# Optimization experiments

Hardware: AMD Instinct MI355X
Metric: run time of the kernel (lower is better)

## Reference

```python
import jax, jax.numpy as jnp
import numpy as np
import math

B, T, C, H = 2, 4096, 512, 8
HD = C // H


def setup_inputs() -> dict:
    key = jax.random.key(0)
    k1, k2, k3 = jax.random.split(key, 3)
    x = jax.random.normal(k1, (B, T, C), dtype=jnp.float32)
    # weights stored as [in, out] so y = x @ W (equivalent to torch Linear with W^T)
    w_qkv = jax.random.normal(k2, (C, 3 * C), dtype=jnp.float32) * (1.0 / math.sqrt(C))
    w_out = jax.random.normal(k3, (C, C), dtype=jnp.float32) * (1.0 / math.sqrt(C))
    return {"x": x, "w_qkv": w_qkv, "w_out": w_out}


def reference(x, w_qkv, w_out):
    Bs, Ts, Cs = x.shape
    qkv = x @ w_qkv                                   # [B,T,3C]
    q, k, v = jnp.split(qkv, 3, axis=-1)
    # [B,H,T,HD]
    q = q.reshape(Bs, Ts, H, HD).transpose(0, 2, 1, 3)
    k = k.reshape(Bs, Ts, H, HD).transpose(0, 2, 1, 3)
    v = v.reshape(Bs, Ts, H, HD).transpose(0, 2, 1, 3)
    scores = jnp.einsum("bhqd,bhkd->bhqk", q, k) / math.sqrt(HD)
    causal = jnp.tril(jnp.ones((Ts, Ts), dtype=bool))
    scores = jnp.where(causal[None, None], scores, -jnp.inf)
    attn = jax.nn.softmax(scores, axis=-1)            # [B,H,T,T]
    out = jnp.einsum("bhqk,bhkd->bhqd", attn, v)      # [B,H,T,HD]
    out = out.transpose(0, 2, 1, 3).reshape(Bs, Ts, Cs)
    return out @ w_out
```

## Files before the change

kernel.cpp:

```cpp
#include <hip/hip_runtime.h>
#include <hip/hip_bf16.h>

typedef __bf16 bf16;
typedef __bf16 bf16x4 __attribute__((ext_vector_type(4)));
typedef __bf16 bf16x8 __attribute__((ext_vector_type(8)));
typedef float f32x4 __attribute__((ext_vector_type(4)));

#define BB 2
#define TT 4096
#define CC 512
#define HH 8
#define HD 64
#define BHD 16
#define M_TOT 8192

#define SCL (0.125f * 1.44269504f)

#if __has_builtin(__builtin_amdgcn_exp2f)
#define EXP2F(x) __builtin_amdgcn_exp2f(x)
#else
#define EXP2F(x) exp2f(x)
#endif

#define GLDS(gptr, lptr)                                                     \
  __builtin_amdgcn_global_load_lds(                                          \
      (const __attribute__((address_space(1))) void*)(gptr),                 \
      (__attribute__((address_space(3))) void*)(lptr), 16, 0, 0)

__global__ __launch_bounds__(256) void convert_x_kernel(
    const float* __restrict__ X, bf16* __restrict__ Xb) {
  const size_t i0 = ((size_t)blockIdx.x * 256 + threadIdx.x) * 16;
  const float4* p = (const float4*)(X + i0);
#pragma unroll
  for (int c = 0; c < 2; ++c) {
    float4 a = p[c * 2], b = p[c * 2 + 1];
    bf16x8 v;
    v[0] = (bf16)a.x; v[1] = (bf16)a.y; v[2] = (bf16)a.z; v[3] = (bf16)a.w;
    v[4] = (bf16)b.x; v[5] = (bf16)b.y; v[6] = (bf16)b.z; v[7] = (bf16)b.w;
    *(bf16x8*)&Xb[i0 + c * 8] = v;
  }
}

__global__ __launch_bounds__(256) void transpose_w_kernel(
    const float* __restrict__ Wq, const float* __restrict__ Wo,
    bf16* __restrict__ WQT, bf16* __restrict__ WOT) {
  __shared__ float tile[64][65];
  int b = blockIdx.x;
  const float* W; bf16* WT; int N, n0, k0;
  if (b < 192) { W = Wq; WT = WQT; N = 1536; n0 = (b % 24) * 64; k0 = (b / 24) * 64; }
  else { b -= 192; W = Wo; WT = WOT; N = 512; n0 = (b & 7) * 64; k0 = (b >> 3) * 64; }
  const int t = threadIdx.x;
  const int rr = t >> 4, cc4 = (t & 15) * 4;
#pragma unroll
  for (int i = 0; i < 4; ++i) {
    float4 v = *(const float4*)&W[(size_t)(k0 + rr + i * 16) * N + n0 + cc4];
    tile[rr + i * 16][cc4 + 0] = v.x;
    tile[rr + i * 16][cc4 + 1] = v.y;
    tile[rr + i * 16][cc4 + 2] = v.z;
    tile[rr + i * 16][cc4 + 3] = v.w;
  }
  __syncthreads();
#pragma unroll
  for (int i = 0; i < 4; ++i) {
    const int nn = rr + i * 16;
    bf16x4 o;
#pragma unroll
    for (int j = 0; j < 4; ++j) o[j] = (bf16)tile[cc4 + j][nn];
    *(bf16x4*)&WT[(size_t)(n0 + nn) * 512 + k0 + cc4] = o;
  }
}

__global__ __launch_bounds__(256) void gemm_qkv_kernel(
    const bf16* __restrict__ Xb, const bf16* __restrict__ Wt,
    bf16* __restrict__ qw, bf16* __restrict__ kw, bf16* __restrict__ vw) {
  __shared__ __align__(16) bf16 As[128 * 64];
  __shared__ __align__(16) bf16 Bs[128 * 64];
  const int tid = threadIdx.x;
  const int wid = tid >> 6, lane = tid & 63, ln = lane & 15, hi = lane >> 4;
  const int wr = wid >> 1, wc = wid & 1;
  const int m0 = blockIdx.x * 128, n0 = blockIdx.y * 128;
  const int srow = lane >> 3, srcc = (lane & 7) ^ srow;

  f32x4 acc[4][4] = {};

  for (int k0 = 0; k0 < 512; k0 += 64) {
    __syncthreads();
#pragma unroll
    for (int i = 0; i < 4; ++i) {
      const int rb = 32 * wid + 8 * i;
      GLDS(&Xb[(size_t)(m0 + rb + srow) * 512 + k0 + srcc * 8], &As[rb * 64]);
      GLDS(&Wt[(size_t)(n0 + rb + srow) * 512 + k0 + srcc * 8], &Bs[rb * 64]);
    }
    __syncthreads();

    bf16x8 af[4][2], bfr[4][2];
#pragma unroll
    for (int mi = 0; mi < 4; ++mi) {
      const int row = wr * 64 + mi * 16 + ln, rs = row & 7;
      af[mi][0] = *(const bf16x8*)&As[row * 64 + ((hi ^ rs) * 8)];
      af[mi][1] = *(const bf16x8*)&As[row * 64 + (((4 + hi) ^ rs) * 8)];
    }
#pragma unroll
    for (int ni = 0; ni < 4; ++ni) {
      const int row = wc * 64 + ni * 16 + ln, rs = row & 7;
      bfr[ni][0] = *(const bf16x8*)&Bs[row * 64 + ((hi ^ rs) * 8)];
      bfr[ni][1] = *(const bf16x8*)&Bs[row * 64 + (((4 + hi) ^ rs) * 8)];
    }
#pragma unroll
    for (int mi = 0; mi < 4; ++mi)
#pragma unroll
      for (int ni = 0; ni < 4; ++ni) {
        acc[mi][ni] = __builtin_amdgcn_mfma_f32_16x16x32_bf16(af[mi][0], bfr[ni][0], acc[mi][ni], 0, 0, 0);
        acc[mi][ni] = __builtin_amdgcn_mfma_f32_16x16x32_bf16(af[mi][1], bfr[ni][1], acc[mi][ni], 0, 0, 0);
      }
  }

#pragma unroll
  for (int mi = 0; mi < 4; ++mi) {
    int rowb = m0 + wr * 64 + mi * 16 + hi * 4;
    int b = rowb >> 12, t0 = rowb & 4095;
#pragma unroll
    for (int ni = 0; ni < 4; ++ni) {
      int n = n0 + wc * 64 + ni * 16 + ln;
      int which = n >> 9, c = n & 511, h = c >> 6, d = c & 63;
      if (which == 2) {
        bf16x4 pv;
#pragma unroll
        for (int r = 0; r < 4; ++r) pv[r] = (bf16)acc[mi][ni][r];
        const int tb = t0 & 63;
        const int paddr = (((tb >> 4) & 1) << 2) | (((tb >> 2) & 3) << 3) |
                          ((tb >> 5) << 5);
        *(bf16x4*)&vw[((size_t)(b * HH + h) * HD + d) * TT + (t0 & ~63) + paddr] = pv;
      } else {
        bf16* dst = which ? kw : qw;
        const float sc = which ? 1.0f : SCL;
#pragma unroll
        for (int r = 0; r < 4; ++r)
          dst[((size_t)(b * HH + h) * TT + t0 + r) * HD + d] = (bf16)(acc[mi][ni][r] * sc);
      }
    }
  }
}

__global__ __launch_bounds__(512, 4) void attn_piece_kernel(
    const bf16* __restrict__ qw, const bf16* __restrict__ kw,
    const bf16* __restrict__ vt,
    bf16* __restrict__ po, float* __restrict__ pl) {
  __shared__ __align__(16) bf16 Ks[2][64 * 64];
  __shared__ __align__(16) bf16 Vs[2][64 * 64];
  const int tid = threadIdx.x;
  const int wid = tid >> 6, lane = tid & 63, ln = lane & 15, hi = lane >> 4;

  int qb4, bh, chunk;
  {
    const int pid = blockIdx.x;
#define MAPB(OFF, K) { const int l = pid - (OFF);                            \
      qb4 = (2 * (K) - 1) - l / (16 * (K));                                  \
      const int r = l % (16 * (K)); bh = r / (K); chunk = r % (K); }
    if      (pid < 256)  MAPB(0, 8)
    else if (pid < 480)  MAPB(256, 7)
    else if (pid < 672)  MAPB(480, 6)
    else if (pid < 832)  MAPB(672, 5)
    else if (pid < 960)  MAPB(832, 4)
    else if (pid < 1056) MAPB(960, 3)
    else if (pid < 1120) MAPB(1056, 2)
    else                 MAPB(1120, 1)
#undef MAPB
  }
  const int ntot = 4 * qb4 + 4;
  const int t0c = chunk * 8;
  const int t1 = (t0c + 8 < ntot) ? (t0c + 8) : ntot;
  const int pid = blockIdx.x;

  const int q0w = qb4 * 256 + wid * 32;

  const int rbase = 8 * wid + (lane >> 3);
  const int srcch = (lane & 7) ^ (lane >> 3);
  const size_t kb = (size_t)bh * TT * HD, vb = (size_t)bh * HD * TT;

  bf16x8 qf[2][2];
#pragma unroll
  for (int qi = 0; qi < 2; ++qi)
#pragma unroll
    for (int h = 0; h < 2; ++h)
      qf[qi][h] = *(const bf16x8*)&qw[((size_t)bh * TT + q0w + qi * 16 + ln) * HD + h * 32 + hi * 8];

  const bf16* kp[4][2];
#pragma unroll
  for (int kt = 0; kt < 4; ++kt) {
    const int krow = kt * 16 + ln;
    kp[kt][0] = &Ks[0][krow * 64 + ((hi ^ (ln & 7)) * 8)];
    kp[kt][1] = &Ks[0][krow * 64 + (((4 + hi) ^ (ln & 7)) * 8)];
  }
  const bf16* vp[4][2];
#pragma unroll
  for (int db = 0; db < 4; ++db) {
    const int d = db * 16 + ln, rowb = d * 64, dx = d & 7;
#pragma unroll
    for (int h2 = 0; h2 < 2; ++h2)
      vp[db][h2] = &Vs[0][rowb + (((4 * h2 + hi) ^ dx) * 8)];
  }

  f32x4 o[2][4] = {};
  f32x4 osum[2] = {};

  bf16x8 vones;
#pragma unroll
  for (int j = 0; j < 8; ++j) vones[j] = (bf16)1.0f;

  {
    const int kv = t0c * 64;
    GLDS(kw + kb + (size_t)(kv + rbase) * HD + srcch * 8, &Ks[0][(8 * wid) * 64]);
    GLDS(vt + vb + (size_t)rbase * TT + kv + srcch * 8, &Vs[0][(8 * wid) * 64]);
  }
  const bf16* pk0 = kw + kb + (size_t)((t0c + 1) * 64 + rbase) * HD + srcch * 8;
  const bf16* pv0 = vt + vb + (size_t)rbase * TT + (t0c + 1) * 64 + srcch * 8;
  __syncthreads();

#define TILE(t_, BUF) do {                                                   \
    const int kv0 = (t_) * 64;                                               \
    if ((t_) + 1 < t1) {                                                     \
      GLDS(pk0, &Ks[(BUF) ^ 1][(8 * wid) * 64]);                             \
      GLDS(pv0, &Vs[(BUF) ^ 1][(8 * wid) * 64]);                             \
      pk0 += (size_t)64 * HD; pv0 += 64;                                     \
    }                                                                        \
    if (kv0 <= q0w + 31) {                                                   \
      f32x4 s[2][4];                                                         \
      __builtin_amdgcn_s_setprio(1);                                         \
      _Pragma("unroll")                                                      \
      for (int kt = 0; kt < 4; ++kt) {                                       \
        bf16x8 kf0 = *(const bf16x8*)(kp[kt][0] + (BUF) * 4096);             \
        bf16x8 kf1 = *(const bf16x8*)(kp[kt][1] + (BUF) * 4096);             \
        _Pragma("unroll")                                                    \
        for (int qi = 0; qi < 2; ++qi) {                                     \
          f32x4 a = {};                                                      \
          a = __builtin_amdgcn_mfma_f32_16x16x32_bf16(kf0, qf[qi][0], a, 0, 0, 0); \
          a = __builtin_amdgcn_mfma_f32_16x16x32_bf16(kf1, qf[qi][1], a, 0, 0, 0); \
          s[qi][kt] = a;                                                     \
        }                                                                    \
      }                                                                      \
      __builtin_amdgcn_s_setprio(0);                                         \
      _Pragma("unroll")                                                      \
      for (int qi = 0; qi < 2; ++qi) {                                       \
        if (kv0 + 63 > q0w + qi * 16) {                                      \
          const int qg = q0w + qi * 16 + ln;                                 \
          _Pragma("unroll")                                                  \
          for (int kt = 0; kt < 4; ++kt)                                     \
            _Pragma("unroll")                                                \
            for (int r = 0; r < 4; ++r)                                      \
              if (kv0 + kt * 16 + hi * 4 + r > qg) s[qi][kt][r] = -1e30f;    \
        }                                                                    \
      }                                                                      \
      _Pragma("unroll")                                                      \
      for (int qi = 0; qi < 2; ++qi)                                         \
        _Pragma("unroll")                                                    \
        for (int kt = 0; kt < 4; ++kt)                                       \
          _Pragma("unroll")                                                  \
          for (int r = 0; r < 4; ++r) s[qi][kt][r] = EXP2F(s[qi][kt][r]);    \
      bf16x8 pa[2][2];                                                       \
      _Pragma("unroll")                                                      \
      for (int qi = 0; qi < 2; ++qi)                                         \
        _Pragma("unroll")                                                    \
        for (int h2 = 0; h2 < 2; ++h2)                                       \
          _Pragma("unroll")                                                  \
          for (int j = 0; j < 8; ++j)                                        \
            pa[qi][h2][j] = (bf16)s[qi][h2 * 2 + (j >> 2)][j & 3];           \
      __builtin_amdgcn_s_setprio(1);                                         \
      _Pragma("unroll")                                                      \
      for (int qi = 0; qi < 2; ++qi) {                                       \
        osum[qi] = __builtin_amdgcn_mfma_f32_16x16x32_bf16(pa[qi][0], vones, osum[qi], 0, 0, 0); \
        osum[qi] = __builtin_amdgcn_mfma_f32_16x16x32_bf16(pa[qi][1], vones, osum[qi], 0, 0, 0); \
      }                                                                      \
      _Pragma("unroll")                                                      \
      for (int db = 0; db < 4; ++db) {                                       \
        _Pragma("unroll")                                                    \
        for (int h2 = 0; h2 < 2; ++h2) {                                     \
          bf16x8 vf = *(const bf16x8*)(vp[db][h2] + (BUF) * 4096);           \
          _Pragma("unroll")                                                  \
          for (int qi = 0; qi < 2; ++qi)                                     \
            o[qi][db] = __builtin_amdgcn_mfma_f32_16x16x32_bf16(pa[qi][h2], vf, o[qi][db], 0, 0, 0); \
        }                                                                    \
      }                                                                      \
      __builtin_amdgcn_s_setprio(0);                                         \
    }                                                                        \
    __syncthreads();                                                         \
  } while (0)

  int t = t0c;
  for (; t + 1 < t1; t += 2) { TILE(t, 0); TILE(t + 1, 1); }
  if (t < t1) TILE(t, 0);

  {
    bf16* ob = po + (size_t)pid * 16384;
#pragma unroll
    for (int qi = 0; qi < 2; ++qi)
#pragma unroll
      for (int db = 0; db < 4; ++db)
#pragma unroll
        for (int r = 0; r < 4; ++r)
          ob[(wid * 32 + qi * 16 + hi * 4 + r) * 64 + db * 16 + ln] = (bf16)o[qi][db][r];
    if (ln == 0) {
#pragma unroll
      for (int qi = 0; qi < 2; ++qi)
#pragma unroll
        for (int r = 0; r < 4; ++r)
          pl[pid * 256 + wid * 32 + qi * 16 + hi * 4 + r] = osum[qi][r];
    }
  }
#undef TILE
}

__global__ __launch_bounds__(256) void attn_combine_kernel(
    const bf16* __restrict__ po, const float* __restrict__ pl,
    bf16* __restrict__ aw) {
  const int cb = blockIdx.x;
  const int qb4 = 15 - (cb >> 5);
  const int r5 = cb & 31;
  const int bh = r5 >> 1, half = r5 & 1;
  const int tid = threadIdx.x;
  const int q_ = half * 128 + (tid >> 1), dc = (tid & 1) * 32;

  const int k = (qb4 + 2) >> 1;
  static const int OFF[9] = {0, 1120, 1056, 960, 832, 672, 480, 256, 0};
  const int p0 = OFF[k] + ((2 * k - 1) - qb4) * 16 * k + bh * k;

  float sum = 0.f;
  for (int c = 0; c < k; ++c) sum += pl[(p0 + c) * 256 + q_];
  const float inv = 1.0f / sum;

  float acc[32] = {};
  for (int c = 0; c < k; ++c) {
    const bf16* ob = po + (size_t)(p0 + c) * 16384 + q_ * 64 + dc;
#pragma unroll
    for (int cc = 0; cc < 4; ++cc) {
      bf16x8 x = *(const bf16x8*)&ob[cc * 8];
#pragma unroll
      for (int j = 0; j < 8; ++j) acc[cc * 8 + j] += (float)x[j];
    }
  }
  bf16* dst = aw + ((size_t)bh * TT + qb4 * 256 + q_) * 64 + dc;
#pragma unroll
  for (int cc = 0; cc < 4; ++cc) {
    bf16x8 outv;
#pragma unroll
    for (int j = 0; j < 8; ++j) outv[j] = (bf16)(acc[cc * 8 + j] * inv);
    *(bf16x8*)&dst[cc * 8] = outv;
  }
}

__global__ __launch_bounds__(256) void gemm_out_kernel(
    const bf16* __restrict__ A, const bf16* __restrict__ Wot,
    float* __restrict__ out) {
  __shared__ __align__(16) bf16 As[128 * 64];
  __shared__ __align__(16) bf16 Bs[64 * 64];
  const int tid = threadIdx.x;
  const int wid = tid >> 6, lane = tid & 63, ln = lane & 15, hi = lane >> 4;
  const int wr = wid >> 1, wc = wid & 1;
  const int m0 = blockIdx.x * 128, n0 = blockIdx.y * 64;
  const int srow = lane >> 3, srcc = (lane & 7) ^ srow;

  f32x4 acc[4][2] = {};

  for (int k0 = 0; k0 < 512; k0 += 64) {
    const int h = k0 >> 6;
    __syncthreads();
#pragma unroll
    for (int i = 0; i < 4; ++i) {
      const int rb = 32 * wid + 8 * i;
      const int m = m0 + rb + srow;
      const int b = m >> 12, t = m & 4095;
      GLDS(&A[((size_t)(b * HH + h) * TT + t) * HD + srcc * 8], &As[rb * 64]);
    }
#pragma unroll
    for (int i = 0; i < 2; ++i) {
      const int rb = 16 * wid + 8 * i;
      GLDS(&Wot[(size_t)(n0 + rb + srow) * 512 + k0 + srcc * 8], &Bs[rb * 64]);
    }
    __syncthreads();

    bf16x8 af[4][2], bfr[2][2];
#pragma unroll
    for (int mi = 0; mi < 4; ++mi) {
      const int row = wr * 64 + mi * 16 + ln, rs = row & 7;
      af[mi][0] = *(const bf16x8*)&As[row * 64 + ((hi ^ rs) * 8)];
      af[mi][1] = *(const bf16x8*)&As[row * 64 + (((4 + hi) ^ rs) * 8)];
    }
#pragma unroll
    for (int ni = 0; ni < 2; ++ni) {
      const int row = wc * 32 + ni * 16 + ln, rs = row & 7;
      bfr[ni][0] = *(const bf16x8*)&Bs[row * 64 + ((hi ^ rs) * 8)];
      bfr[ni][1] = *(const bf16x8*)&Bs[row * 64 + (((4 + hi) ^ rs) * 8)];
    }
#pragma unroll
    for (int mi = 0; mi < 4; ++mi)
#pragma unroll
      for (int ni = 0; ni < 2; ++ni) {
        acc[mi][ni] = __builtin_amdgcn_mfma_f32_16x16x32_bf16(af[mi][0], bfr[ni][0], acc[mi][ni], 0, 0, 0);
        acc[mi][ni] = __builtin_amdgcn_mfma_f32_16x16x32_bf16(af[mi][1], bfr[ni][1], acc[mi][ni], 0, 0, 0);
      }
  }

#pragma unroll
  for (int mi = 0; mi < 4; ++mi) {
    int rowb = m0 + wr * 64 + mi * 16 + hi * 4;
#pragma unroll
    for (int ni = 0; ni < 2; ++ni) {
      int n = n0 + wc * 32 + ni * 16 + ln;
#pragma unroll
      for (int r = 0; r < 4; ++r)
        out[(size_t)(rowb + r) * 512 + n] = acc[mi][ni][r];
    }
  }
}

extern "C" void kernel_launch(void* const* d_in, const int* in_sizes, int n_in,
                              void* d_out, int out_size, void* d_ws, size_t ws_size,
                              hipStream_t stream) {
  const float* x = (const float*)d_in[0];
  const float* w_qkv = (const float*)d_in[1];
  const float* w_out = (const float*)d_in[2];
  float* out = (float*)d_out;

  const size_t QKV_ELEMS = (size_t)BHD * TT * HD;
  bf16* qw = (bf16*)d_ws;
  bf16* kw = qw + QKV_ELEMS;
  bf16* vw = kw + QKV_ELEMS;
  bf16* aw = vw + QKV_ELEMS;
  bf16* po = aw + QKV_ELEMS;
  float* pl = (float*)(po + (size_t)1152 * 16384);
  bf16* wqt = (bf16*)(pl + (size_t)1152 * 256);
  bf16* wot = wqt + (size_t)1536 * 512;
  bf16* xb = po;

  convert_x_kernel<<<1024, 256, 0, stream>>>(x, xb);
  transpose_w_kernel<<<256, 256, 0, stream>>>(w_qkv, w_out, wqt, wot);
  gemm_qkv_kernel<<<dim3(M_TOT / 128, 1536 / 128), 256, 0, stream>>>(xb, wqt, qw, kw, vw);
  attn_piece_kernel<<<1152, 512, 0, stream>>>(qw, kw, vw, po, pl);
  attn_combine_kernel<<<512, 256, 0, stream>>>(po, pl, aw);
  gemm_out_kernel<<<dim3(M_TOT / 128, 512 / 64), 256, 0, stream>>>(aw, wot, out);
}
```

Measured before the change: 111.6 us.

## Drop LDS staging in attention; waves load K/V directly with independent work mapping

The attention piece kernel no longer stages K/V tiles in shared memory behind barriers. Each wave now loads its K and V fragments straight from global memory (relying on L2/L1) and runs its own causal loop bound, so waves stop early instead of idling at __syncthreads. Blocks shrink to 4 waves, and a new per-wave mapping spreads work units across heads and query blocks. The cost is redundant global/L2 traffic, since the 8 waves sharing a piece no longer reuse one LDS copy, and loads are not software-pipelined.

```diff
diff --git a/kernel.cpp b/kernel.cpp
--- a/kernel.cpp
+++ b/kernel.cpp
@@ -142,40 +142,36 @@
   }
 }
 
-__global__ __launch_bounds__(512, 4) void attn_piece_kernel(
+__global__ __launch_bounds__(256, 4) void attn_piece_kernel(
     const bf16* __restrict__ qw, const bf16* __restrict__ kw,
     const bf16* __restrict__ vt,
     bf16* __restrict__ po, float* __restrict__ pl) {
-  __shared__ __align__(16) bf16 Ks[2][64 * 64];
-  __shared__ __align__(16) bf16 Vs[2][64 * 64];
   const int tid = threadIdx.x;
   const int wid = tid >> 6, lane = tid & 63, ln = lane & 15, hi = lane >> 4;
 
-  int qb4, bh, chunk;
-  {
-    const int pid = blockIdx.x;
-#define MAPB(OFF, K) { const int l = pid - (OFF);                            \
-      qb4 = (2 * (K) - 1) - l / (16 * (K));                                  \
-      const int r = l % (16 * (K)); bh = r / (K); chunk = r % (K); }
-    if      (pid < 256)  MAPB(0, 8)
-    else if (pid < 480)  MAPB(256, 7)
-    else if (pid < 672)  MAPB(480, 6)
-    else if (pid < 832)  MAPB(672, 5)
-    else if (pid < 960)  MAPB(832, 4)
-    else if (pid < 1056) MAPB(960, 3)
-    else if (pid < 1120) MAPB(1056, 2)
-    else                 MAPB(1120, 1)
-#undef MAPB
-  }
+  const int g = blockIdx.x & 7;
+  int u = (blockIdx.x >> 3) * 4 + wid;
+  int bh = g;
+  if (u >= 576) { bh = g + 8; u -= 576; }
+  int qb4 = 15;
+  while (qb4 > 0) {
+    const int cnt = 8 * ((4 * qb4 + 11) >> 3);
+    if (u < cnt) break;
+    u -= cnt;
+    --qb4;
+  }
+  const int chunk = u >> 3, wavein = u & 7;
   const int ntot = 4 * qb4 + 4;
   const int t0c = chunk * 8;
-  const int t1 = (t0c + 8 < ntot) ? (t0c + 8) : ntot;
-  const int pid = blockIdx.x;
-
-  const int q0w = qb4 * 256 + wid * 32;
-
-  const int rbase = 8 * wid + (lane >> 3);
-  const int srcch = (lane & 7) ^ (lane >> 3);
+  const int t1c = (t0c + 8 < ntot) ? (t0c + 8) : ntot;
+  const int q0w = qb4 * 256 + wavein * 32;
+  const int t1w0 = ((q0w + 31) >> 6) + 1;
+  const int t1w = (t1c < t1w0) ? t1c : t1w0;
+
+  const int K = (qb4 + 2) >> 1;
+  static const int OFF[9] = {0, 1120, 1056, 960, 832, 672, 480, 256, 0};
+  const int pid = OFF[K] + ((2 * K - 1) - qb4) * 16 * K + bh * K + chunk;
+
   const size_t kb = (size_t)bh * TT * HD, vb = (size_t)bh * HD * TT;
 
   bf16x8 qf[2][2];
@@ -185,22 +181,6 @@
     for (int h = 0; h < 2; ++h)
       qf[qi][h] = *(const bf16x8*)&qw[((size_t)bh * TT + q0w + qi * 16 + ln) * HD + h * 32 + hi * 8];
 
-  const bf16* kp[4][2];
-#pragma unroll
-  for (int kt = 0; kt < 4; ++kt) {
-    const int krow = kt * 16 + ln;
-    kp[kt][0] = &Ks[0][krow * 64 + ((hi ^ (ln & 7)) * 8)];
-    kp[kt][1] = &Ks[0][krow * 64 + (((4 + hi) ^ (ln & 7)) * 8)];
-  }
-  const bf16* vp[4][2];
-#pragma unroll
-  for (int db = 0; db < 4; ++db) {
-    const int d = db * 16 + ln, rowb = d * 64, dx = d & 7;
-#pragma unroll
-    for (int h2 = 0; h2 < 2; ++h2)
-      vp[db][h2] = &Vs[0][rowb + (((4 * h2 + hi) ^ dx) * 8)];
-  }
-
   f32x4 o[2][4] = {};
   f32x4 osum[2] = {};
 
@@ -208,87 +188,84 @@
 #pragma unroll
   for (int j = 0; j < 8; ++j) vones[j] = (bf16)1.0f;
 
-  {
-    const int kv = t0c * 64;
-    GLDS(kw + kb + (size_t)(kv + rbase) * HD + srcch * 8, &Ks[0][(8 * wid) * 64]);
-    GLDS(vt + vb + (size_t)rbase * TT + kv + srcch * 8, &Vs[0][(8 * wid) * 64]);
-  }
-  const bf16* pk0 = kw + kb + (size_t)((t0c + 1) * 64 + rbase) * HD + srcch * 8;
-  const bf16* pv0 = vt + vb + (size_t)rbase * TT + (t0c + 1) * 64 + srcch * 8;
-  __syncthreads();
-
-#define TILE(t_, BUF) do {                                                   \
-    const int kv0 = (t_) * 64;                                               \
-    if ((t_) + 1 < t1) {                                                     \
-      GLDS(pk0, &Ks[(BUF) ^ 1][(8 * wid) * 64]);                             \
-      GLDS(pv0, &Vs[(BUF) ^ 1][(8 * wid) * 64]);                             \
-      pk0 += (size_t)64 * HD; pv0 += 64;                                     \
-    }                                                                        \
-    if (kv0 <= q0w + 31) {                                                   \
-      f32x4 s[2][4];                                                         \
-      __builtin_amdgcn_s_setprio(1);                                         \
-      _Pragma("unroll")                                                      \
-      for (int kt = 0; kt < 4; ++kt) {                                       \
-        bf16x8 kf0 = *(const bf16x8*)(kp[kt][0] + (BUF) * 4096);             \
-        bf16x8 kf1 = *(const bf16x8*)(kp[kt][1] + (BUF) * 4096);             \
-        _Pragma("unroll")                                                    \
-        for (int qi = 0; qi < 2; ++qi) {                                     \
-          f32x4 a = {};                                                      \
-          a = __builtin_amdgcn_mfma_f32_16x16x32_bf16(kf0, qf[qi][0], a, 0, 0, 0); \
-          a = __builtin_amdgcn_mfma_f32_16x16x32_bf16(kf1, qf[qi][1], a, 0, 0, 0); \
-          s[qi][kt] = a;                                                     \
-        }                                                                    \
-      }                                                                      \
-      __builtin_amdgcn_s_setprio(0);                                         \
-      _Pragma("unroll")                                                      \
-      for (int qi = 0; qi < 2; ++qi) {                                       \
-        if (kv0 + 63 > q0w + qi * 16) {                                      \
-          const int qg = q0w + qi * 16 + ln;                                 \
-          _Pragma("unroll")                                                  \
-          for (int kt = 0; kt < 4; ++kt)                                     \
-            _Pragma("unroll")                                                \
-            for (int r = 0; r < 4; ++r)                                      \
-              if (kv0 + kt * 16 + hi * 4 + r > qg) s[qi][kt][r] = -1e30f;    \
-        }                                                                    \
-      }                                                                      \
-      _Pragma("unroll")                                                      \
-      for (int qi = 0; qi < 2; ++qi)                                         \
-        _Pragma("unroll")                                                    \
-        for (int kt = 0; kt < 4; ++kt)                                       \
-          _Pragma("unroll")                                                  \
-          for (int r = 0; r < 4; ++r) s[qi][kt][r] = EXP2F(s[qi][kt][r]);    \
-      bf16x8 pa[2][2];                                                       \
-      _Pragma("unroll")                                                      \
-      for (int qi = 0; qi < 2; ++qi)                                         \
-        _Pragma("unroll")                                                    \
-        for (int h2 = 0; h2 < 2; ++h2)                                       \
-          _Pragma("unroll")                                                  \
-          for (int j = 0; j < 8; ++j)                                        \
-            pa[qi][h2][j] = (bf16)s[qi][h2 * 2 + (j >> 2)][j & 3];           \
-      __builtin_amdgcn_s_setprio(1);                                         \
-      _Pragma("unroll")                                                      \
-      for (int qi = 0; qi < 2; ++qi) {                                       \
-        osum[qi] = __builtin_amdgcn_mfma_f32_16x16x32_bf16(pa[qi][0], vones, osum[qi], 0, 0, 0); \
-        osum[qi] = __builtin_amdgcn_mfma_f32_16x16x32_bf16(pa[qi][1], vones, osum[qi], 0, 0, 0); \
-      }                                                                      \
-      _Pragma("unroll")                                                      \
-      for (int db = 0; db < 4; ++db) {                                       \
-        _Pragma("unroll")                                                    \
-        for (int h2 = 0; h2 < 2; ++h2) {                                     \
-          bf16x8 vf = *(const bf16x8*)(vp[db][h2] + (BUF) * 4096);           \
-          _Pragma("unroll")                                                  \
-          for (int qi = 0; qi < 2; ++qi)                                     \
-            o[qi][db] = __builtin_amdgcn_mfma_f32_16x16x32_bf16(pa[qi][h2], vf, o[qi][db], 0, 0, 0); \
-        }                                                                    \
-      }                                                                      \
-      __builtin_amdgcn_s_setprio(0);                                         \
-    }                                                                        \
-    __syncthreads();                                                         \
-  } while (0)
-
-  int t = t0c;
-  for (; t + 1 < t1; t += 2) { TILE(t, 0); TILE(t + 1, 1); }
-  if (t < t1) TILE(t, 0);
+  const bf16* kptr = kw + kb + (size_t)(t0c * 64 + ln) * HD + hi * 8;
+  const bf16* vptr[4];
+#pragma unroll
+  for (int db = 0; db < 4; ++db)
+    vptr[db] = vt + vb + (size_t)(db * 16 + ln) * TT + t0c * 64 + hi * 8;
+
+  for (int t = t0c; t < t1w; ++t) {
+    const int kv0 = t * 64;
+    bf16x8 kf0[4], kf1[4];
+#pragma unroll
+    for (int kt = 0; kt < 4; ++kt) {
+      kf0[kt] = *(const bf16x8*)(kptr + kt * 1024);
+      kf1[kt] = *(const bf16x8*)(kptr + kt * 1024 + 32);
+    }
+    bf16x8 vf[4][2];
+#pragma unroll
+    for (int db = 0; db < 4; ++db)
+#pragma unroll
+      for (int h2 = 0; h2 < 2; ++h2)
+        vf[db][h2] = *(const bf16x8*)(vptr[db] + h2 * 32);
+    kptr += 4096;
+#pragma unroll
+    for (int db = 0; db < 4; ++db) vptr[db] += 64;
+
+    f32x4 s[2][4];
+    __builtin_amdgcn_s_setprio(1);
+#pragma unroll
+    for (int kt = 0; kt < 4; ++kt)
+#pragma unroll
+      for (int qi = 0; qi < 2; ++qi) {
+        f32x4 a = {};
+        a = __builtin_amdgcn_mfma_f32_16x16x32_bf16(kf0[kt], qf[qi][0], a, 0, 0, 0);
+        a = __builtin_amdgcn_mfma_f32_16x16x32_bf16(kf1[kt], qf[qi][1], a, 0, 0, 0);
+        s[qi][kt] = a;
+      }
+    __builtin_amdgcn_s_setprio(0);
+
+#pragma unroll
+    for (int qi = 0; qi < 2; ++qi) {
+      if (kv0 + 63 > q0w + qi * 16) {
+        const int qg = q0w + qi * 16 + ln;
+#pragma unroll
+        for (int kt = 0; kt < 4; ++kt)
+#pragma unroll
+          for (int r = 0; r < 4; ++r)
+            if (kv0 + kt * 16 + hi * 4 + r > qg) s[qi][kt][r] = -1e30f;
+      }
+    }
+#pragma unroll
+    for (int qi = 0; qi < 2; ++qi)
+#pragma unroll
+      for (int kt = 0; kt < 4; ++kt)
+#pragma unroll
+        for (int r = 0; r < 4; ++r) s[qi][kt][r] = EXP2F(s[qi][kt][r]);
+    bf16x8 pa[2][2];
+#pragma unroll
+    for (int qi = 0; qi < 2; ++qi)
+#pragma unroll
+      for (int h2 = 0; h2 < 2; ++h2)
+#pragma unroll
+        for (int j = 0; j < 8; ++j)
+          pa[qi][h2][j] = (bf16)s[qi][h2 * 2 + (j >> 2)][j & 3];
+
+    __builtin_amdgcn_s_setprio(1);
+#pragma unroll
+    for (int qi = 0; qi < 2; ++qi) {
+      osum[qi] = __builtin_amdgcn_mfma_f32_16x16x32_bf16(pa[qi][0], vones, osum[qi], 0, 0, 0);
+      osum[qi] = __builtin_amdgcn_mfma_f32_16x16x32_bf16(pa[qi][1], vones, osum[qi], 0, 0, 0);
+    }
+#pragma unroll
+    for (int db = 0; db < 4; ++db)
+#pragma unroll
+      for (int h2 = 0; h2 < 2; ++h2)
+#pragma unroll
+        for (int qi = 0; qi < 2; ++qi)
+          o[qi][db] = __builtin_amdgcn_mfma_f32_16x16x32_bf16(pa[qi][h2], vf[db][h2], o[qi][db], 0, 0, 0);
+    __builtin_amdgcn_s_setprio(0);
+  }
 
   {
     bf16* ob = po + (size_t)pid * 16384;
@@ -298,16 +275,15 @@
       for (int db = 0; db < 4; ++db)
 #pragma unroll
         for (int r = 0; r < 4; ++r)
-          ob[(wid * 32 + qi * 16 + hi * 4 + r) * 64 + db * 16 + ln] = (bf16)o[qi][db][r];
+          ob[(wavein * 32 + qi * 16 + hi * 4 + r) * 64 + db * 16 + ln] = (bf16)o[qi][db][r];
     if (ln == 0) {
 #pragma unroll
       for (int qi = 0; qi < 2; ++qi)
 #pragma unroll
         for (int r = 0; r < 4; ++r)
-          pl[pid * 256 + wid * 32 + qi * 16 + hi * 4 + r] = osum[qi][r];
-    }
-  }
-#undef TILE
+          pl[pid * 256 + wavein * 32 + qi * 16 + hi * 4 + r] = osum[qi][r];
+    }
+  }
 }
 
 __global__ __launch_bounds__(256) void attn_combine_kernel(
@@ -435,7 +411,7 @@
   convert_x_kernel<<<1024, 256, 0, stream>>>(x, xb);
   transpose_w_kernel<<<256, 256, 0, stream>>>(w_qkv, w_out, wqt, wot);
   gemm_qkv_kernel<<<dim3(M_TOT / 128, 1536 / 128), 256, 0, stream>>>(xb, wqt, qw, kw, vw);
-  attn_piece_kernel<<<1152, 512, 0, stream>>>(qw, kw, vw, po, pl);
+  attn_piece_kernel<<<2304, 256, 0, stream>>>(qw, kw, vw, po, pl);
   attn_combine_kernel<<<512, 256, 0, stream>>>(po, pl, aw);
   gemm_out_kernel<<<dim3(M_TOT / 128, 512 / 64), 256, 0, stream>>>(aw, wot, out);
 }
```

New measurement: 330.0 us. 2.96x slower.
